# Performance work log

Measured on AMD Instinct MI355X. Metric: run time of the kernel, lower is better.

The kernel has to match this reference:

```python
import jax, jax.numpy as jnp
import numpy as np

N = 50000
E = 1_600_000
SIGMA = 0.5


def _spmm(rows, cols, vals, dense):
    # sparse [N,N] @ dense [N,D] via gather + segment_sum
    return jax.ops.segment_sum(vals[:, None] * dense[cols], rows, num_segments=N)


def _gnn_layer(h, rows, cols, vals, W, active=True):
    support = h @ W            # [N, out]
    out = _spmm(rows, cols, vals, support)
    return jax.nn.relu(out) if active else out


def setup_inputs() -> dict:
    key = jax.random.key(0)
    ks = jax.random.split(key, 14)
    dims = [512, 500, 500, 2000, 10, 10]  # n_input, enc1, enc2, enc3, n_z, n_clusters
    inp = {
        "x": jax.random.normal(ks[0], (N, dims[0]), dtype=jnp.float32),
        "adj_rows": jax.random.randint(ks[1], (E,), 0, N, dtype=jnp.int32),
        "adj_cols": jax.random.randint(ks[2], (E,), 0, N, dtype=jnp.int32),
        "adj_vals": jax.random.uniform(ks[3], (E,), dtype=jnp.float32),
        "tra1": jax.random.normal(ks[4], (N, dims[1]), dtype=jnp.float32),
        "tra2": jax.random.normal(ks[5], (N, dims[2]), dtype=jnp.float32),
        "tra3": jax.random.normal(ks[6], (N, dims[3]), dtype=jnp.float32),
        "z": jax.random.normal(ks[7], (N, dims[4]), dtype=jnp.float32),
    }
    for i in range(5):
        fan_in, fan_out = dims[i], dims[i + 1]
        bound = float(np.sqrt(6.0 / (fan_in + fan_out)))  # xavier uniform
        inp[f"W{i+1}"] = jax.random.uniform(
            ks[8 + i], (fan_in, fan_out), dtype=jnp.float32, minval=-bound, maxval=bound)
    return inp


def reference(x, adj_rows, adj_cols, adj_vals, tra1, tra2, tra3, z,
              W1, W2, W3, W4, W5):
    s = SIGMA
    h = _gnn_layer(x, adj_rows, adj_cols, adj_vals, W1)
    h = _gnn_layer((1 - s) * h + s * tra1, adj_rows, adj_cols, adj_vals, W2)
    h = _gnn_layer((1 - s) * h + s * tra2, adj_rows, adj_cols, adj_vals, W3)
    h = _gnn_layer((1 - s) * h + s * tra3, adj_rows, adj_cols, adj_vals, W4)
    h = _gnn_layer((1 - s) * h + s * z, adj_rows, adj_cols, adj_vals, W5, active=False)
    return h
```

## Files before the change

kernel.cpp:

```cpp
#include <hip/hip_runtime.h>
#include <hip/hip_bf16.h>


#define SCAN_CHUNK 512
#define BM 128
#define BN 128
#define BK 64
#define NSLICE 8

typedef __attribute__((ext_vector_type(4))) float f32x4;
typedef __attribute__((ext_vector_type(8))) __bf16 bf16x8;
typedef __attribute__((ext_vector_type(8))) short s16x8;

__device__ __forceinline__ bf16x8 as_bf(s16x8 v) { union { s16x8 s; bf16x8 b; } u; u.s = v; return u.b; }
__device__ __forceinline__ ushort f2bf(float f) {
    uint u = __float_as_uint(f);
    return (ushort)((u + 0x7FFFu + ((u >> 16) & 1u)) >> 16);
}
__device__ __forceinline__ float bf2f(ushort s) { return __uint_as_float(((uint)s) << 16); }

#define GLL16(g, l)                                                                 \
    __builtin_amdgcn_global_load_lds((const __attribute__((address_space(1))) void*)(g), \
                                     (__attribute__((address_space(3))) void*)(l), 16, 0, 0)

#define STAGE_TILE8(k0, base)                                                       \
    _Pragma("unroll")                                                               \
    for (int i = 0; i < 2; ++i) {                                                   \
        int ar = row0 + arow_off + i * 64;                                          \
        if (ar >= M) ar = M - 1;                                                    \
        GLL16(A + (size_t)ar * 512 + (k0) + acol, &lds[(base) + (w * 8 + i * 64) * BK]); \
        GLL16(Bt + (size_t)(col0 + arow_off + i * 64) * 512 + (k0) + acol,          \
              &lds[(base) + 8192 + (w * 8 + i * 64) * BK]);                         \
    }

#define COMPUTE_TILE8(base)                                                         \
    _Pragma("unroll")                                                               \
    for (int s = 0; s < 2; ++s) {                                                   \
        int cswz = (((s * 4 + (l >> 4)) ^ (l & 7)) << 3);                           \
        bf16x8 af[4], bfr[2];                                                       \
        _Pragma("unroll")                                                           \
        for (int m = 0; m < 4; ++m)                                                 \
            af[m] = as_bf(*(const s16x8*)&lds[(base) + (wr + m * 16 + (l & 15)) * BK + cswz]); \
        _Pragma("unroll")                                                           \
        for (int n = 0; n < 2; ++n)                                                 \
            bfr[n] = as_bf(*(const s16x8*)&lds[(base) + 8192 + (wc + n * 16 + (l & 15)) * BK + cswz]); \
        _Pragma("unroll")                                                           \
        for (int m = 0; m < 4; ++m)                                                 \
            _Pragma("unroll")                                                       \
            for (int n = 0; n < 2; ++n)                                             \
                acc[m][n] = __builtin_amdgcn_mfma_f32_16x16x32_bf16(af[m], bfr[n], acc[m][n], 0, 0, 0); \
    }

#define KLOOP_PIPELINED()                                                           \
    STAGE_TILE8(0, 0);                                                              \
    int base = 0;                                                                   \
    _Pragma("unroll 1")                                                             \
    for (int t = 0; t < 8; ++t) {                                                   \
        if (t < 7) {                                                                \
            STAGE_TILE8((t + 1) * BK, base ^ 16384);                                \
            asm volatile("s_waitcnt vmcnt(4)" ::: "memory");                        \
        } else {                                                                    \
            asm volatile("s_waitcnt vmcnt(0)" ::: "memory");                        \
        }                                                                           \
        __builtin_amdgcn_s_barrier();                                               \
        __builtin_amdgcn_sched_barrier(0);                                          \
        COMPUTE_TILE8(base);                                                        \
        __builtin_amdgcn_sched_barrier(0);                                          \
        __builtin_amdgcn_s_barrier();                                               \
        base ^= 16384;                                                              \
    }

__global__ __launch_bounds__(512) void gemm_sup(const ushort* __restrict__ A,
                                                const ushort* __restrict__ Bt,
                                                ushort* __restrict__ C, int M) {
    __shared__ ushort lds[32768];
    int tid = threadIdx.x;
    int w = tid >> 6, l = tid & 63;
    int row0 = blockIdx.y * BM, col0 = blockIdx.x * BN;
    int wr = (w >> 2) * 64, wc = (w & 3) * 32;
    f32x4 acc[4][2] = {};
    int arow_off = w * 8 + (l >> 3);
    int acol = (((l & 7) ^ (l >> 3)) << 3);

    KLOOP_PIPELINED();

    int crow = (l >> 4) * 4, ccol = l & 15;
#pragma unroll
    for (int m = 0; m < 4; ++m)
#pragma unroll
        for (int n = 0; n < 2; ++n) {
            int gc = col0 + wc + n * 16 + ccol;
#pragma unroll
            for (int r = 0; r < 4; ++r) {
                int gr = row0 + wr + m * 16 + crow + r;
                if (gr < M) C[(size_t)gr * 512 + gc] = f2bf(acc[m][n][r]);
            }
        }
}

__global__ __launch_bounds__(512) void gemm3_w4(const ushort* __restrict__ A,
                                                const ushort* __restrict__ Bt,
                                                const float* __restrict__ T,
                                                const float* __restrict__ W4,
                                                float* __restrict__ sup4p, int M) {
    __shared__ ushort lds[32768];
    int tid = threadIdx.x;
    int w = tid >> 6, l = tid & 63;
    int row0 = blockIdx.y * BM, col0 = blockIdx.x * BN;
    int wr = (w >> 2) * 64, wc = (w & 3) * 32;
    int crow = (l >> 4) * 4, ccol = l & 15;

    bf16x8 w4f;
    {
        s16x8 tmp;
#pragma unroll
        for (int kk = 0; kk < 8; ++kk) {
            int gk = col0 + (w & 3) * 32 + ((l >> 4) << 3) + kk;
            float v = (ccol < 10 && gk < 2000) ? 0.5f * W4[(size_t)gk * 10 + ccol] : 0.f;
            tmp[kk] = (short)f2bf(v);
        }
        w4f = as_bf(tmp);
    }

    f32x4 acc[4][2] = {};
    int arow_off = w * 8 + (l >> 3);
    int acol = (((l & 7) ^ (l >> 3)) << 3);

    KLOOP_PIPELINED();

    ushort* actS = lds;

    __syncthreads();
#pragma unroll
    for (int m = 0; m < 4; ++m)
#pragma unroll
        for (int n = 0; n < 2; ++n) {
            int cl = wc + n * 16 + ccol;
            int cch = cl >> 3, clo = cl & 7;
#pragma unroll
            for (int r = 0; r < 4; ++r) {
                int rl = wr + m * 16 + crow + r;
                actS[rl * 128 + (((cch ^ (rl & 7)) << 3) | clo)] = f2bf(fmaxf(acc[m][n][r], 0.f));
            }
        }
    __syncthreads();

    f32x4 acc2[4] = {};
    {
        int chunk = (w & 3) * 4 + (l >> 4);
#pragma unroll
        for (int m = 0; m < 4; ++m) {
            int row = wr + m * 16 + ccol;
            bf16x8 af = as_bf(*(const s16x8*)&actS[row * 128 + ((chunk ^ (row & 7)) << 3)]);
            acc2[m] = __builtin_amdgcn_mfma_f32_16x16x32_bf16(af, w4f, acc2[m], 0, 0, 0);
        }
    }
    __syncthreads();

    {
        int r_off = tid >> 5;
        int c4 = (tid & 31) * 4;
        int chunk = (tid & 31) >> 1;
        int lo = (tid & 1) * 4;
#pragma unroll
        for (int p = 0; p < 8; ++p) {
            int rl = p * 16 + r_off;
            int gr = row0 + rl;
            int gcb = col0 + c4;
            ushort4 h;
            if (gr < M && gcb + 3 < 2000) {
                float4 tv = *(const float4*)(T + (size_t)gr * 2000 + gcb);
                h.x = f2bf(tv.x); h.y = f2bf(tv.y); h.z = f2bf(tv.z); h.w = f2bf(tv.w);
            } else {
                float e[4];
#pragma unroll
                for (int i = 0; i < 4; ++i)
                    e[i] = (gr < M && gcb + i < 2000) ? T[(size_t)gr * 2000 + gcb + i] : 0.f;
                h.x = f2bf(e[0]); h.y = f2bf(e[1]); h.z = f2bf(e[2]); h.w = f2bf(e[3]);
            }
            *(ushort4*)&actS[rl * 128 + ((chunk ^ (rl & 7)) << 3) + lo] = h;
        }
    }
    __syncthreads();

    {
        int chunk = (w & 3) * 4 + (l >> 4);
#pragma unroll
        for (int m = 0; m < 4; ++m) {
            int row = wr + m * 16 + ccol;
            bf16x8 af = as_bf(*(const s16x8*)&actS[row * 128 + ((chunk ^ (row & 7)) << 3)]);
            acc2[m] = __builtin_amdgcn_mfma_f32_16x16x32_bf16(af, w4f, acc2[m], 0, 0, 0);
        }
    }
    __syncthreads();

    float* redS = (float*)lds;
    {
        int q = w & 3;
#pragma unroll
        for (int m = 0; m < 4; ++m)
#pragma unroll
            for (int r = 0; r < 4; ++r) {
                int row = wr + m * 16 + crow + r;
                redS[(q * 128 + row) * 16 + ccol] = acc2[m][r];
            }
    }
    __syncthreads();
    {
        float* dst = sup4p + (size_t)blockIdx.x * ((size_t)M * 10);
#pragma unroll
        for (int p = 0; p < 4; ++p) {
            int o = p * 512 + tid;
            int row = o >> 4, col = o & 15;
            int gr = row0 + row;
            if (col < 10 && gr < M) {
                float s = redS[(0 * 128 + row) * 16 + col] + redS[(1 * 128 + row) * 16 + col]
                        + redS[(2 * 128 + row) * 16 + col] + redS[(3 * 128 + row) * 16 + col];
                dst[(size_t)gr * 10 + col] = s;
            }
        }
    }
}

__global__ __launch_bounds__(256) void sup4_reduce(const float* __restrict__ P,
                                                   float* __restrict__ O, int n) {
    int i = blockIdx.x * 256 + threadIdx.x;
    if (i >= n) return;
    float s = 0.f;
#pragma unroll
    for (int j = 0; j < 16; ++j) s += P[(size_t)j * n + i];
    O[i] = s;
}

__global__ __launch_bounds__(256) void cvt4(const float* __restrict__ s,
                                            ushort* __restrict__ d, long n4) {
    long i = (long)blockIdx.x * 256 + threadIdx.x;
    if (i >= n4) return;
    float4 v = ((const float4*)s)[i];
    ushort4 o = { f2bf(v.x), f2bf(v.y), f2bf(v.z), f2bf(v.w) };
    ((ushort4*)d)[i] = o;
}

__global__ __launch_bounds__(256) void cvt_wt(const float* __restrict__ W,
                                              ushort* __restrict__ Wt,
                                              int Ksrc, int Nsrc, int Npad) {
    int i = blockIdx.x * 256 + threadIdx.x;
    if (i >= Npad * 512) return;
    int n = i >> 9, k = i & 511;
    float v = (k < Ksrc && n < Nsrc) ? W[(size_t)k * Nsrc + n] : 0.f;
    Wt[i] = f2bf(v);
}

__global__ __launch_bounds__(256) void csr_count(const int* __restrict__ rows,
                                                 int* __restrict__ cnt, int E) {
    int e = blockIdx.x * 256 + threadIdx.x;
    if (e < E) atomicAdd(&cnt[rows[e]], 1);
}

__global__ __launch_bounds__(256) void scan1(const int* __restrict__ cnt,
                                             int* __restrict__ csum, int n) {
    __shared__ int red[256];
    int base = blockIdx.x * SCAN_CHUNK;
    int t = threadIdx.x;
    int s = 0;
    if (base + t < n) s += cnt[base + t];
    if (base + t + 256 < n) s += cnt[base + t + 256];
    red[t] = s;
    __syncthreads();
    for (int off = 128; off; off >>= 1) {
        if (t < off) red[t] += red[t + off];
        __syncthreads();
    }
    if (t == 0) csum[blockIdx.x] = red[0];
}

__global__ void scan2(int* csum, int nch) {
    if (threadIdx.x == 0 && blockIdx.x == 0) {
        int acc = 0;
        for (int i = 0; i < nch; ++i) { int v = csum[i]; csum[i] = acc; acc += v; }
    }
}

__global__ __launch_bounds__(256) void scan3(const int* __restrict__ cnt,
                                             const int* __restrict__ csum,
                                             int* __restrict__ rowptr, int n, int E) {
    __shared__ int sm[SCAN_CHUNK];
    int base = blockIdx.x * SCAN_CHUNK;
    int t = threadIdx.x;
    for (int i = t; i < SCAN_CHUNK; i += 256) sm[i] = (base + i < n) ? cnt[base + i] : 0;
    __syncthreads();
    for (int off = 1; off < SCAN_CHUNK; off <<= 1) {
        int i0 = t, i1 = t + 256;
        int v0 = (i0 >= off) ? sm[i0 - off] : 0;
        int v1 = (i1 >= off) ? sm[i1 - off] : 0;
        __syncthreads();
        sm[i0] += v0;
        sm[i1] += v1;
        __syncthreads();
    }
    int off0 = csum[blockIdx.x];
    for (int i = t; i < SCAN_CHUNK; i += 256)
        if (base + i < n) rowptr[base + i] = off0 + (i ? sm[i - 1] : 0);
    if (blockIdx.x == 0 && t == 0) rowptr[n] = E;
}

__global__ __launch_bounds__(256) void csr_fill(const int* __restrict__ rows,
                                                const int* __restrict__ cols,
                                                const float* __restrict__ vals,
                                                int* __restrict__ cur,
                                                int2* __restrict__ edges, int E) {
    int e = blockIdx.x * 256 + threadIdx.x;
    if (e >= E) return;
    int p = atomicAdd(&cur[rows[e]], 1);
    edges[p] = make_int2(cols[e], __float_as_int(vals[e]));
}

__global__ __launch_bounds__(256) void spmm_bfs(const int* __restrict__ rowptr,
                                                const int2* __restrict__ edges,
                                                const ushort* __restrict__ S,
                                                const float* __restrict__ T,
                                                ushort* __restrict__ O,
                                                int nrows, int domix) {
    int wid = (int)((blockIdx.x * 256 + threadIdx.x) >> 6);
    if (wid >= nrows) return;
    int lane = threadIdx.x & 63;
    int g = lane >> 3, t = lane & 7;
    int c0 = blockIdx.y * 64 + t * 8;
    int beg = rowptr[wid], end = rowptr[wid + 1];

    float acc[8] = {0.f, 0.f, 0.f, 0.f, 0.f, 0.f, 0.f, 0.f};
    int e = beg + g;
    for (; e + 8 < end; e += 16) {
        int2 e0 = edges[e], e1 = edges[e + 8];
        float v0 = __int_as_float(e0.y), v1 = __int_as_float(e1.y);
        s16x8 a = *(const s16x8*)(S + (size_t)e0.x * 512 + c0);
        s16x8 b = *(const s16x8*)(S + (size_t)e1.x * 512 + c0);
#pragma unroll
        for (int j = 0; j < 8; ++j)
            acc[j] += v0 * bf2f((ushort)a[j]) + v1 * bf2f((ushort)b[j]);
    }
    if (e < end) {
        int2 e0 = edges[e];
        float v0 = __int_as_float(e0.y);
        s16x8 a = *(const s16x8*)(S + (size_t)e0.x * 512 + c0);
#pragma unroll
        for (int j = 0; j < 8; ++j)
            acc[j] += v0 * bf2f((ushort)a[j]);
    }

#pragma unroll
    for (int off = 8; off <= 32; off <<= 1)
#pragma unroll
        for (int j = 0; j < 8; ++j)
            acc[j] += __shfl_xor(acc[j], off, 64);

    if (g != 0) return;
    float res[8];
    if (domix) {
        float tv[8] = {0.f, 0.f, 0.f, 0.f, 0.f, 0.f, 0.f, 0.f};
        const float* trow = T + (size_t)wid * 500;
        if (c0 + 8 <= 500) {
            float4 t0 = *(const float4*)(trow + c0);
            float4 t1 = *(const float4*)(trow + c0 + 4);
            tv[0] = t0.x; tv[1] = t0.y; tv[2] = t0.z; tv[3] = t0.w;
            tv[4] = t1.x; tv[5] = t1.y; tv[6] = t1.z; tv[7] = t1.w;
        } else {
#pragma unroll
            for (int j = 0; j < 8; ++j)
                if (c0 + j < 500) tv[j] = trow[c0 + j];
        }
#pragma unroll
        for (int j = 0; j < 8; ++j)
            res[j] = (c0 + j < 500) ? (0.5f * fmaxf(acc[j], 0.f) + 0.5f * tv[j]) : 0.f;
    } else {
#pragma unroll
        for (int j = 0; j < 8; ++j)
            res[j] = (c0 + j < 500) ? acc[j] : 0.f;
    }
    s16x8 o;
#pragma unroll
    for (int j = 0; j < 8; ++j) o[j] = (short)f2bf(res[j]);
    *(s16x8*)(O + (size_t)wid * 512 + c0) = o;
}

__global__ __launch_bounds__(256) void spmm10(const int* __restrict__ rowptr,
                                              const int2* __restrict__ edges,
                                              const float* __restrict__ S,
                                              const float* __restrict__ T,
                                              const float* __restrict__ W5,
                                              float* __restrict__ O, int nrows) {
    int g = (int)((blockIdx.x * 256 + threadIdx.x) >> 4);
    int t = threadIdx.x & 15;
    if (g >= nrows || t >= 10) return;
    int beg = rowptr[g], end = rowptr[g + 1];
    float acc = 0.f;
    for (int e = beg; e < end; ++e) {
        int2 ed = edges[e];
        acc += __int_as_float(ed.y) * S[(size_t)ed.x * 10 + t];
    }
    if (W5) {
        float m = 0.5f * fmaxf(acc, 0.f) + 0.5f * T[(size_t)g * 10 + t];
        float s5 = 0.f;
#pragma unroll
        for (int i = 0; i < 10; ++i)
            s5 += __shfl(m, i, 16) * W5[i * 10 + t];
        O[(size_t)g * 10 + t] = s5;
    } else {
        O[(size_t)g * 10 + t] = acc;
    }
}

extern "C" void kernel_launch(void* const* d_in, const int* in_sizes, int n_in,
                              void* d_out, int out_size, void* d_ws, size_t ws_size,
                              hipStream_t stream) {
    const float* x    = (const float*)d_in[0];
    const int*   ar   = (const int*)d_in[1];
    const int*   ac   = (const int*)d_in[2];
    const float* av   = (const float*)d_in[3];
    const float* tra1 = (const float*)d_in[4];
    const float* tra2 = (const float*)d_in[5];
    const float* tra3 = (const float*)d_in[6];
    const float* z    = (const float*)d_in[7];
    const float* W1   = (const float*)d_in[8];
    const float* W2   = (const float*)d_in[9];
    const float* W3   = (const float*)d_in[10];
    const float* W4   = (const float*)d_in[11];
    const float* W5   = (const float*)d_in[12];

    const int E = in_sizes[1];
    const int N = in_sizes[7] / 10;
    const int NCH = (N + SCAN_CHUNK - 1) / SCAN_CHUNK;

    ushort* Abf    = (ushort*)d_ws;
    ushort* Sbf    = Abf + (size_t)N * 512;
    ushort* Wt1    = Sbf + (size_t)N * 512;
    ushort* Wt2    = Wt1 + 512 * 512;
    ushort* Wt3    = Wt2 + 512 * 512;
    float*  sup4   = (float*)(Wt3 + 2048 * 512);
    float*  sup5   = sup4 + (size_t)N * 10;
    float*  sup4p  = sup5 + (size_t)N * 10;
    int2*   edges  = (int2*)(sup4p + (size_t)16 * N * 10);
    int*    rowptr = (int*)(edges + E);
    int*    cnt    = rowptr + (N + 1);
    int*    csum   = cnt + N;
    float*  out    = (float*)d_out;

    dim3 blk(256);
    dim3 blk8(512);

    cvt4<<<(int)(((long)N * 512 / 4 + 255) / 256), blk, 0, stream>>>(x, Abf, (long)N * 512 / 4);
    cvt_wt<<<(512 * 512 + 255) / 256, blk, 0, stream>>>(W1, Wt1, 512, 500, 512);
    cvt_wt<<<(512 * 512 + 255) / 256, blk, 0, stream>>>(W2, Wt2, 500, 500, 512);
    cvt_wt<<<(2048 * 512 + 255) / 256, blk, 0, stream>>>(W3, Wt3, 500, 2000, 2048);

    hipMemsetAsync(cnt, 0, (size_t)N * sizeof(int), stream);
    csr_count<<<(E + 255) / 256, blk, 0, stream>>>(ar, cnt, E);
    scan1<<<NCH, blk, 0, stream>>>(cnt, csum, N);
    scan2<<<1, 64, 0, stream>>>(csum, NCH);
    scan3<<<NCH, blk, 0, stream>>>(cnt, csum, rowptr, N, E);
    hipMemcpyAsync(cnt, rowptr, (size_t)N * sizeof(int), hipMemcpyDeviceToDevice, stream);
    csr_fill<<<(E + 255) / 256, blk, 0, stream>>>(ar, ac, av, cnt, edges, E);

    dim3 spmm_grid((N * 64 + 255) / 256, NSLICE);
    const int spmm10_blocks = (N * 16 + 255) / 256;

    {
        dim3 g(4, (N + BM - 1) / BM);
        gemm_sup<<<g, blk8, 0, stream>>>(Abf, Wt1, Sbf, N);
    }
    spmm_bfs<<<spmm_grid, blk, 0, stream>>>(rowptr, edges, Sbf, tra1, Abf, N, 1);

    {
        dim3 g(4, (N + BM - 1) / BM);
        gemm_sup<<<g, blk8, 0, stream>>>(Abf, Wt2, Sbf, N);
    }
    spmm_bfs<<<spmm_grid, blk, 0, stream>>>(rowptr, edges, Sbf, tra2, Abf, N, 1);

    spmm_bfs<<<spmm_grid, blk, 0, stream>>>(rowptr, edges, Abf, nullptr, Sbf, N, 0);
    {
        dim3 g(16, (N + BM - 1) / BM);
        gemm3_w4<<<g, blk8, 0, stream>>>(Sbf, Wt3, tra3, W4, sup4p, N);
    }
    sup4_reduce<<<(N * 10 + 255) / 256, blk, 0, stream>>>(sup4p, sup4, N * 10);

    spmm10<<<spmm10_blocks, blk, 0, stream>>>(rowptr, edges, sup4, z, W5, sup5, N);

    spmm10<<<spmm10_blocks, blk, 0, stream>>>(rowptr, edges, sup5, nullptr, nullptr, out, N);
}
```

Before: 1.363 ms.

## Map eight lanes per row in bf16 SpMM instead of a full wavefront

Result: faster. 1.246 ms (-8.5%).

```diff
diff --git a/kernel.cpp b/kernel.cpp
--- a/kernel.cpp
+++ b/kernel.cpp
@@ -321,44 +321,41 @@
                                                 const float* __restrict__ T,
                                                 ushort* __restrict__ O,
                                                 int nrows, int domix) {
-    int wid = (int)((blockIdx.x * 256 + threadIdx.x) >> 6);
-    if (wid >= nrows) return;
-    int lane = threadIdx.x & 63;
-    int g = lane >> 3, t = lane & 7;
+    int row = (int)((blockIdx.x * 256 + threadIdx.x) >> 3);
+    if (row >= nrows) return;
+    int t = threadIdx.x & 7;
     int c0 = blockIdx.y * 64 + t * 8;
-    int beg = rowptr[wid], end = rowptr[wid + 1];
+    int beg = rowptr[row], end = rowptr[row + 1];
+    const ushort* Sc = S + c0;
 
     float acc[8] = {0.f, 0.f, 0.f, 0.f, 0.f, 0.f, 0.f, 0.f};
-    int e = beg + g;
-    for (; e + 8 < end; e += 16) {
-        int2 e0 = edges[e], e1 = edges[e + 8];
+    int e = beg;
+    for (; e + 3 < end; e += 4) {
+        int2 e0 = edges[e], e1 = edges[e + 1], e2 = edges[e + 2], e3 = edges[e + 3];
         float v0 = __int_as_float(e0.y), v1 = __int_as_float(e1.y);
-        s16x8 a = *(const s16x8*)(S + (size_t)e0.x * 512 + c0);
-        s16x8 b = *(const s16x8*)(S + (size_t)e1.x * 512 + c0);
+        float v2 = __int_as_float(e2.y), v3 = __int_as_float(e3.y);
+        s16x8 a = *(const s16x8*)(Sc + (size_t)e0.x * 512);
+        s16x8 b = *(const s16x8*)(Sc + (size_t)e1.x * 512);
+        s16x8 c = *(const s16x8*)(Sc + (size_t)e2.x * 512);
+        s16x8 d = *(const s16x8*)(Sc + (size_t)e3.x * 512);
 #pragma unroll
         for (int j = 0; j < 8; ++j)
-            acc[j] += v0 * bf2f((ushort)a[j]) + v1 * bf2f((ushort)b[j]);
-    }
-    if (e < end) {
+            acc[j] += v0 * bf2f((ushort)a[j]) + v1 * bf2f((ushort)b[j])
+                    + v2 * bf2f((ushort)c[j]) + v3 * bf2f((ushort)d[j]);
+    }
+    for (; e < end; ++e) {
         int2 e0 = edges[e];
         float v0 = __int_as_float(e0.y);
-        s16x8 a = *(const s16x8*)(S + (size_t)e0.x * 512 + c0);
+        s16x8 a = *(const s16x8*)(Sc + (size_t)e0.x * 512);
 #pragma unroll
         for (int j = 0; j < 8; ++j)
             acc[j] += v0 * bf2f((ushort)a[j]);
     }
 
-#pragma unroll
-    for (int off = 8; off <= 32; off <<= 1)
-#pragma unroll
-        for (int j = 0; j < 8; ++j)
-            acc[j] += __shfl_xor(acc[j], off, 64);
-
-    if (g != 0) return;
     float res[8];
     if (domix) {
         float tv[8] = {0.f, 0.f, 0.f, 0.f, 0.f, 0.f, 0.f, 0.f};
-        const float* trow = T + (size_t)wid * 500;
+        const float* trow = T + (size_t)row * 500;
         if (c0 + 8 <= 500) {
             float4 t0 = *(const float4*)(trow + c0);
             float4 t1 = *(const float4*)(trow + c0 + 4);
@@ -380,7 +377,7 @@
     s16x8 o;
 #pragma unroll
     for (int j = 0; j < 8; ++j) o[j] = (short)f2bf(res[j]);
-    *(s16x8*)(O + (size_t)wid * 512 + c0) = o;
+    *(s16x8*)(O + (size_t)row * 512 + c0) = o;
 }
 
 __global__ __launch_bounds__(256) void spmm10(const int* __restrict__ rowptr,
@@ -461,7 +458,7 @@
     hipMemcpyAsync(cnt, rowptr, (size_t)N * sizeof(int), hipMemcpyDeviceToDevice, stream);
     csr_fill<<<(E + 255) / 256, blk, 0, stream>>>(ar, ac, av, cnt, edges, E);
 
-    dim3 spmm_grid((N * 64 + 255) / 256, NSLICE);
+    dim3 spmm_grid((N * 8 + 255) / 256, NSLICE);
     const int spmm10_blocks = (N * 16 + 255) / 256;
 
     {
```
